# Kernel optimization log

Measured on AMD Instinct MI355X. Metric: run time of the kernel, lower is better.

## Reference

```python
import jax, jax.numpy as jnp
import numpy as np
import math

D = 1024
H = 16
DH = D // H


def sinusoidal_pe(length, d):
    pos = jnp.arange(length, dtype=jnp.float32)[:, None]            # [S,1]
    div = jnp.exp(jnp.arange(0, d, 2, dtype=jnp.float32) * (-math.log(10000.0) / d))  # [d/2]
    ang = pos * div                                                  # [S,d/2]
    # interleave sin (even idx) and cos (odd idx)
    return jnp.stack([jnp.sin(ang), jnp.cos(ang)], axis=-1).reshape(length, d)


def setup_inputs() -> dict:
    key = jax.random.key(0)
    ks = jax.random.split(key, 12)
    s = 0.02
    x = jax.random.normal(ks[0], (2, 2048, D), dtype=jnp.float32)
    return {
        "x": x,
        "ln_g": jnp.ones((D,), jnp.float32),
        "ln_b": jnp.zeros((D,), jnp.float32),
        "Wq": jax.random.normal(ks[1], (D, D), jnp.float32) * s,
        "bq": jnp.zeros((D,), jnp.float32),
        "Wk": jax.random.normal(ks[2], (D, D), jnp.float32) * s,
        "bk": jnp.zeros((D,), jnp.float32),
        "Wv": jax.random.normal(ks[3], (D, D), jnp.float32) * s,
        "bv": jnp.zeros((D,), jnp.float32),
        "Wp": jax.random.normal(ks[4], (D, D), jnp.float32) * s,
        "Wo": jax.random.normal(ks[5], (D, D), jnp.float32) * s,
        "bo": jnp.zeros((D,), jnp.float32),
        "u_bias": jax.random.normal(ks[6], (H, DH), jnp.float32) * 0.05,
        "v_bias": jax.random.normal(ks[7], (H, DH), jnp.float32) * 0.05,
    }


def _relative_shift(pos_score):
    # pos_score: [B,H,S,S]
    B, Hh, S1, S2 = pos_score.shape
    padded = jnp.concatenate([jnp.zeros((B, Hh, S1, 1), pos_score.dtype), pos_score], axis=-1)
    padded = padded.reshape(B, Hh, S2 + 1, S1)
    return padded[:, :, 1:].reshape(B, Hh, S1, S2)


def reference(x, ln_g, ln_b, Wq, bq, Wk, bk, Wv, bv, Wp, Wo, bo, u_bias, v_bias):
    B, S, Dm = x.shape
    dh = Dm // H
    scale = dh ** -0.5

    pe = sinusoidal_pe(S, Dm)                                        # [S,D]

    mu = jnp.mean(x, axis=-1, keepdims=True)
    var = jnp.var(x, axis=-1, keepdims=True)
    xn = (x - mu) / jnp.sqrt(var + 1e-5) * ln_g + ln_b

    q = (xn @ Wq + bq).reshape(B, S, H, dh)                          # [B,S,H,dh]
    k = (xn @ Wk + bk).reshape(B, S, H, dh)
    v = (xn @ Wv + bv).reshape(B, S, H, dh)
    p = (pe @ Wp).reshape(S, H, dh)                                  # [S,H,dh]

    content = jnp.einsum('bihd,bjhd->bhij', q + u_bias, k)
    pos = jnp.einsum('bihd,jhd->bhij', q + v_bias, p)
    pos = _relative_shift(pos)

    attn = jax.nn.softmax((content + pos) * scale, axis=-1)          # [B,H,S,S]
    head = jnp.einsum('bhij,bjhd->bihd', attn, v).reshape(B, S, Dm)
    return head @ Wo + bo
```

## Files before the change

### kernel.cpp

```cpp
#include <hip/hip_runtime.h>
#include <hip/hip_bf16.h>
#include <math.h>

#define Dm   1024
#define Hh   16
#define Sx   2048

typedef short s16x8 __attribute__((ext_vector_type(8)));
typedef float f32x4 __attribute__((ext_vector_type(4)));
typedef unsigned short u16;
typedef u16 u16x4 __attribute__((ext_vector_type(4)));

#if defined(__has_builtin)
#  if __has_builtin(__builtin_amdgcn_cvt_pk_bf16_f32)
#    define HAVE_PKBF16 1
typedef __bf16 bfv2 __attribute__((ext_vector_type(2)));
#  endif
#  if __has_builtin(__builtin_amdgcn_exp2f)
#    define EXP2(x) __builtin_amdgcn_exp2f(x)
#  endif
#endif
#ifndef EXP2
#  define EXP2(x) exp2f(x)
#endif

#define ATT_SCALE 0.1803368801111204f

__device__ __forceinline__ float wave_sum64(float v) {
#pragma unroll
    for (int o = 32; o > 0; o >>= 1) v += __shfl_xor(v, o, 64);
    return v;
}
__device__ __forceinline__ u16 f2bf(float x) {
    unsigned int u = __float_as_uint(x);
    unsigned int r = u + 0x7FFFu + ((u >> 16) & 1u);
    return (u16)(r >> 16);
}
__device__ __forceinline__ float bf2f(u16 h) {
    return __uint_as_float(((unsigned int)h) << 16);
}

__global__ __launch_bounds__(256) void ln_kernel(const float* __restrict__ x,
                                                 const float* __restrict__ g,
                                                 const float* __restrict__ b,
                                                 u16* __restrict__ out16) {
    int row = blockIdx.x;
    int tid = threadIdx.x;
    const float4* xr = (const float4*)(x + (size_t)row * Dm);
    float4 v = xr[tid];
    float s  = v.x + v.y + v.z + v.w;
    float ss = v.x * v.x + v.y * v.y + v.z * v.z + v.w * v.w;
    __shared__ float rbuf[8];
    s  = wave_sum64(s);
    ss = wave_sum64(ss);
    if ((tid & 63) == 0) { rbuf[tid >> 6] = s; rbuf[4 + (tid >> 6)] = ss; }
    __syncthreads();
    float mean = (rbuf[0] + rbuf[1] + rbuf[2] + rbuf[3]) * (1.0f / Dm);
    float msq  = (rbuf[4] + rbuf[5] + rbuf[6] + rbuf[7]) * (1.0f / Dm);
    float var  = msq - mean * mean;
    float rstd = 1.0f / sqrtf(var + 1e-5f);
    float4 gg = ((const float4*)g)[tid];
    float4 bb = ((const float4*)b)[tid];
    float o[4];
    o[0] = (v.x - mean) * rstd * gg.x + bb.x;
    o[1] = (v.y - mean) * rstd * gg.y + bb.y;
    o[2] = (v.z - mean) * rstd * gg.z + bb.z;
    o[3] = (v.w - mean) * rstd * gg.w + bb.w;
    u16x4 hi, lo;
#pragma unroll
    for (int i = 0; i < 4; i++) {
        u16 h = f2bf(o[i]);
        hi[i] = h;
        lo[i] = f2bf(o[i] - bf2f(h));
    }
    *(u16x4*)&out16[(size_t)row * 2048 + tid * 4]        = hi;
    *(u16x4*)&out16[(size_t)row * 2048 + 1024 + tid * 4] = lo;
}

__global__ __launch_bounds__(256) void pe_kernel(u16* __restrict__ pe16) {
    int idx = blockIdx.x * 256 + threadIdx.x;
    int r = idx >> 9;
    int t = idx & 511;
    double div = exp((double)(2 * t) * (-9.210340371976184 / 1024.0));
    double ang = (double)r * div;
    float sv = (float)sin(ang), cv = (float)cos(ang);
    u16 sh = f2bf(sv), chh = f2bf(cv);
    u16* row = pe16 + (size_t)r * 2048;
    row[2 * t]            = sh;
    row[2 * t + 1]        = chh;
    row[1024 + 2 * t]     = f2bf(sv - bf2f(sh));
    row[1024 + 2 * t + 1] = f2bf(cv - bf2f(chh));
}

__global__ __launch_bounds__(256) void wconv_kernel(const float* __restrict__ W0,
                                                    const float* __restrict__ W1,
                                                    const float* __restrict__ W2,
                                                    const float* __restrict__ W3,
                                                    const float* __restrict__ W4,
                                                    u16* __restrict__ WT) {
    int wz = blockIdx.z;
    const float* W = (wz == 0) ? W0 : (wz == 1) ? W1 : (wz == 2) ? W2 : (wz == 3) ? W3 : W4;
    u16* T = WT + (size_t)wz * 1024 * 2048;
    __shared__ float tile[32][33];
    int n0 = blockIdx.x * 32, k0 = blockIdx.y * 32;
    int tx = threadIdx.x & 31, ty = threadIdx.x >> 5;
#pragma unroll
    for (int r = 0; r < 32; r += 8)
        tile[ty + r][tx] = W[(size_t)(k0 + ty + r) * 1024 + n0 + tx];
    __syncthreads();
#pragma unroll
    for (int r = 0; r < 32; r += 8) {
        int n = ty + r;
        float x = tile[tx][n];
        u16 h = f2bf(x);
        float rem = x - bf2f(h);
        T[(size_t)(n0 + n) * 2048 + k0 + tx]        = h;
        T[(size_t)(n0 + n) * 2048 + 1024 + k0 + tx] = f2bf(rem);
    }
}

__global__ __launch_bounds__(256, 4) void gemm_bf16x3(const u16* __restrict__ A16,
                                                      const u16* __restrict__ WT,
                                                      const float* __restrict__ bias,
                                                      float cscale,
                                                      float* __restrict__ C,
                                                      u16* __restrict__ Cb, int M) {
    const int K = 1024, N = 1024;
    __shared__ __align__(16) u16 Ah[64 * 72];
    __shared__ __align__(16) u16 Bh[128 * 72];
    int tid = threadIdx.x;
    int bn = blockIdx.x * 128, bm = blockIdx.y * 64;
    int ar = tid >> 2, ac = (tid & 3) * 8;
    int br = tid >> 1, bs = (tid & 1);
    int w = tid >> 6, ln = tid & 63, g = ln >> 4, l15 = ln & 15;
    int wm = (w & 1) * 32, wn = (w >> 1) * 64;

    const u16* Ap = A16 + (size_t)(bm + ar) * 2048 + ac;
    const u16* Bp = WT + (size_t)(bn + br) * 2048 + bs * 1024;
    u16* Aw = &Ah[ar * 72 + ac];
    u16* Bw = &Bh[br * 72 + bs * 32];

    f32x4 acc[2][4] = {};
    s16x8 pah = *(const s16x8*)Ap;
    s16x8 pal = *(const s16x8*)(Ap + 1024);
    s16x8 pb0 = *(const s16x8*)Bp;
    s16x8 pb1 = *(const s16x8*)(Bp + 8);
    s16x8 pb2 = *(const s16x8*)(Bp + 16);
    s16x8 pb3 = *(const s16x8*)(Bp + 24);

    for (int k0 = 0; k0 < K; k0 += 32) {
        __syncthreads();
        *(s16x8*)Aw        = pah;
        *(s16x8*)(Aw + 32) = pal;
        *(s16x8*)Bw        = pb0;
        *(s16x8*)(Bw + 8)  = pb1;
        *(s16x8*)(Bw + 16) = pb2;
        *(s16x8*)(Bw + 24) = pb3;
        int kn = k0 + 32;
        if (kn < K) {
            pah = *(const s16x8*)(Ap + kn);
            pal = *(const s16x8*)(Ap + 1024 + kn);
            pb0 = *(const s16x8*)(Bp + kn);
            pb1 = *(const s16x8*)(Bp + kn + 8);
            pb2 = *(const s16x8*)(Bp + kn + 16);
            pb3 = *(const s16x8*)(Bp + kn + 24);
        }
        __syncthreads();
        s16x8 ah0 = *(const s16x8*)&Ah[(wm + l15) * 72 + g * 8];
        s16x8 al0 = *(const s16x8*)&Ah[(wm + l15) * 72 + 32 + g * 8];
        s16x8 ah1 = *(const s16x8*)&Ah[(wm + 16 + l15) * 72 + g * 8];
        s16x8 al1 = *(const s16x8*)&Ah[(wm + 16 + l15) * 72 + 32 + g * 8];
#pragma unroll
        for (int nt = 0; nt < 4; nt++) {
            int n = (wn + 16 * nt + l15) * 72;
            s16x8 bh = *(const s16x8*)&Bh[n + g * 8];
            s16x8 bl = *(const s16x8*)&Bh[n + 32 + g * 8];
            acc[0][nt] = __builtin_amdgcn_mfma_f32_16x16x32_bf16(ah0, bh, acc[0][nt], 0, 0, 0);
            acc[0][nt] = __builtin_amdgcn_mfma_f32_16x16x32_bf16(al0, bh, acc[0][nt], 0, 0, 0);
            acc[0][nt] = __builtin_amdgcn_mfma_f32_16x16x32_bf16(ah0, bl, acc[0][nt], 0, 0, 0);
            acc[1][nt] = __builtin_amdgcn_mfma_f32_16x16x32_bf16(ah1, bh, acc[1][nt], 0, 0, 0);
            acc[1][nt] = __builtin_amdgcn_mfma_f32_16x16x32_bf16(al1, bh, acc[1][nt], 0, 0, 0);
            acc[1][nt] = __builtin_amdgcn_mfma_f32_16x16x32_bf16(ah1, bl, acc[1][nt], 0, 0, 0);
        }
    }

    float bv[4];
#pragma unroll
    for (int nt = 0; nt < 4; nt++)
        bv[nt] = bias ? bias[bn + wn + 16 * nt + l15] : 0.0f;
#pragma unroll
    for (int mt = 0; mt < 2; mt++)
#pragma unroll
        for (int r = 0; r < 4; r++) {
            int row = bm + wm + 16 * mt + g * 4 + r;
            if (Cb) {
                u16* cp = Cb + (size_t)row * N + bn + wn + l15;
#pragma unroll
                for (int nt = 0; nt < 4; nt++)
                    cp[16 * nt] = f2bf((acc[mt][nt][r] + bv[nt]) * cscale);
            } else {
                float* cp = C + (size_t)row * N + bn + wn + l15;
#pragma unroll
                for (int nt = 0; nt < 4; nt++)
                    cp[16 * nt] = (acc[mt][nt][r] + bv[nt]) * cscale;
            }
        }
}

__global__ __launch_bounds__(256) void vtrans_kernel(const u16* __restrict__ v,
                                                     u16* __restrict__ vT) {
    __shared__ u16 L[32 * 72];
    int jt = blockIdx.x, h = blockIdx.y, b = blockIdx.z;
    int tid = threadIdx.x;
    int row = tid >> 3, cc = tid & 7;
    const u16* src = v + ((size_t)(b * Sx + jt * 32 + row)) * Dm + h * 64 + cc * 8;
    *(s16x8*)&L[row * 72 + cc * 8] = *(const s16x8*)src;
    __syncthreads();
    int d = tid >> 2, jq = tid & 3;
    s16x8 o;
#pragma unroll
    for (int jj = 0; jj < 8; jj++) o[jj] = (short)L[(jq * 8 + jj) * 72 + d];
    u16* dst = vT + (((size_t)(b * 16 + h) * 64 + jt)) * 2048 + d * 32 + jq * 8;
    *(s16x8*)dst = o;
}

__global__ __launch_bounds__(256) void ukvb_kernel(const u16* __restrict__ k,
                                                   const u16* __restrict__ pp,
                                                   const float* __restrict__ u,
                                                   const float* __restrict__ vb,
                                                   float* __restrict__ ukg,
                                                   float* __restrict__ vbg) {
    int jid = blockIdx.x * 256 + threadIdx.x;
    const u16* src; const float* vec; float* dst; int idx;
    if (jid < 2 * Hh * Sx) {
        int j = jid & 2047, h = (jid >> 11) & 15, b = jid >> 15;
        src = k + ((size_t)(b * Sx + j)) * Dm + h * 64;
        vec = u + h * 64; dst = ukg; idx = jid;
    } else {
        int j2 = jid - 2 * Hh * Sx;
        int r = j2 & 2047, h = j2 >> 11;
        src = pp + (size_t)r * Dm + h * 64;
        vec = vb + h * 64; dst = vbg; idx = j2;
    }
    float s = 0.0f;
#pragma unroll
    for (int c = 0; c < 8; c++) {
        s16x8 kk = *(const s16x8*)(src + c * 8);
#pragma unroll
        for (int i = 0; i < 8; i++) s += bf2f((u16)kk[i]) * vec[c * 8 + i];
    }
    dst[idx] = s;
}

__device__ __forceinline__ void wfill2(s16x8 a0, s16x8 a1, const u16* PW,
                                       int g, int l15, f32x4& d0, f32x4& d1) {
    f32x4 z = {0.f, 0.f, 0.f, 0.f};
    s16x8 b00 = *(const s16x8*)&PW[l15 * 72 + g * 8];
    s16x8 b01 = *(const s16x8*)&PW[l15 * 72 + 32 + g * 8];
    s16x8 b10 = *(const s16x8*)&PW[(16 + l15) * 72 + g * 8];
    s16x8 b11 = *(const s16x8*)&PW[(16 + l15) * 72 + 32 + g * 8];
    d0 = __builtin_amdgcn_mfma_f32_16x16x32_bf16(a0, b00, z, 0, 0, 0);
    d0 = __builtin_amdgcn_mfma_f32_16x16x32_bf16(a1, b01, d0, 0, 0, 0);
    d1 = __builtin_amdgcn_mfma_f32_16x16x32_bf16(a0, b10, z, 0, 0, 0);
    d1 = __builtin_amdgcn_mfma_f32_16x16x32_bf16(a1, b11, d1, 0, 0, 0);
}

__device__ __forceinline__ void window_fill(s16x8 aq0, s16x8 aq1, s16x8 ab0, s16x8 ab1,
                                            const u16* PW, float* Ws,
                                            const float* __restrict__ vbb,
                                            int vstart, int sb, int rbase, int g, int l15) {
    f32x4 e0, e1;
    if (vstart + 31 <= Sx) {
        wfill2(aq0, aq1, PW, g, l15, e0, e1);
    } else if (vstart > Sx) {
        wfill2(ab0, ab1, PW, g, l15, e0, e1);
    } else {
        f32x4 d0, d1, f0, f1;
        wfill2(aq0, aq1, PW, g, l15, d0, d1);
        wfill2(ab0, ab1, PW, g, l15, f0, f1);
        int v0 = vstart + l15, v1 = vstart + 16 + l15;
#pragma unroll
        for (int r = 0; r < 4; r++) {
            e0[r] = (v0 > Sx) ? f0[r] : d0[r];
            e1[r] = (v1 > Sx) ? f1[r] : d1[r];
        }
    }
    int v0 = vstart + l15, v1 = vstart + 16 + l15;
    int pc0 = v0 < Sx ? v0 : v0 - Sx - 1;
    int pc1 = v1 < Sx ? v1 : v1 - Sx - 1;
    float vb0 = (v0 == Sx) ? 0.0f : vbb[pc0];
    float vb1 = (v1 == Sx) ? 0.0f : vbb[pc1];
    int bs = sb + rbase;
#pragma unroll
    for (int r = 0; r < 4; r++) {
        int b2 = bs + r; if (b2 >= 96) b2 -= 96;
        int sl0 = b2 + l15; if (sl0 >= 96) sl0 -= 96;
        int sl1 = sl0 + 16; if (sl1 >= 96) sl1 -= 96;
        Ws[(rbase + r) * 98 + sl0] = (v0 == Sx) ? 0.0f : e0[r] + vb0;
        Ws[(rbase + r) * 98 + sl1] = (v1 == Sx) ? 0.0f : e1[r] + vb1;
    }
}

__global__ __launch_bounds__(256, 4) void flash_kernel(const u16* __restrict__ q,
                                                       const u16* __restrict__ k,
                                                       const u16* __restrict__ vt,
                                                       const u16* __restrict__ pp,
                                                       const float* __restrict__ ukg,
                                                       const float* __restrict__ vbg,
                                                       u16* __restrict__ head16) {
    __shared__ __align__(16) unsigned char smem[39424];
    float* Ws = (float*)smem;
    u16*   Qs = (u16*)smem;
    u16*   Kt = (u16*)(smem + 25088);
    u16*   PW = (u16*)(smem + 29696);
    u16*   PA = (u16*)(smem + 34304);

    int tid = threadIdx.x, blk = blockIdx.x;
    int grp = (blk & 7) + 8 * (blk >> 8);
    int it  = (blk >> 3) & 31;
    int h = grp & 15, b = grp >> 4;
    int i0 = it * 64;
    int a0 = 1984 - i0;

    const u16* qb  = q  + ((size_t)b * Sx) * Dm + h * 64;
    const u16* kb  = k  + ((size_t)b * Sx) * Dm + h * 64;
    const u16* vtb = vt + ((size_t)(b * 16 + h) * 64) * 2048;
    const u16* ppb = pp + h * 64;
    const float* ukb = ukg + (size_t)(b * Hh + h) * Sx;
    const float* vbb = vbg + (size_t)h * Sx;

    int w = tid >> 6, ln = tid & 63, g = ln >> 4, l15 = ln & 15;
    int rv = tid >> 3, ch = tid & 7;
    int rbase = 16 * w + 4 * g;

    for (int c = tid; c < 65 * 8; c += 256) {
        int row = c >> 3, cc = c & 7;
        int i = i0 + row;
        s16x8 tv = {0, 0, 0, 0, 0, 0, 0, 0};
        if (i < Sx) tv = *(const s16x8*)(qb + (size_t)i * Dm + cc * 8);
        *(s16x8*)&Qs[row * 72 + cc * 8] = tv;
    }
    __syncthreads();

    s16x8 aq0 = *(const s16x8*)&Qs[(16 * w + l15) * 72 + g * 8];
    s16x8 aq1 = *(const s16x8*)&Qs[(16 * w + l15) * 72 + 32 + g * 8];
    s16x8 ab0 = *(const s16x8*)&Qs[(16 * w + 1 + l15) * 72 + g * 8];
    s16x8 ab1 = *(const s16x8*)&Qs[(16 * w + 1 + l15) * 72 + 32 + g * 8];
    __syncthreads();

    for (int f = 0; f < 3; f++) {
        int vrb = f * 32;
        if (f) __syncthreads();
        {
            int vv = a0 + vrb + rv;
            s16x8 tv = {0, 0, 0, 0, 0, 0, 0, 0};
            if (vv != Sx) {
                int pc = vv < Sx ? vv : vv - Sx - 1;
                tv = *(const s16x8*)(ppb + (size_t)pc * Dm + ch * 8);
            }
            *(s16x8*)&PW[rv * 72 + ch * 8] = tv;
        }
        __syncthreads();
        window_fill(aq0, aq1, ab0, ab1, PW, Ws, vbb, a0 + vrb, vrb, rbase, g, l15);
    }

    f32x4 O[4] = {{0.f,0.f,0.f,0.f},{0.f,0.f,0.f,0.f},{0.f,0.f,0.f,0.f},{0.f,0.f,0.f,0.f}};
    float m_w = -1e30f;
    float l_i[4] = {0.f, 0.f, 0.f, 0.f};
    int wro[4];
#pragma unroll
    for (int r = 0; r < 4; r++) wro[r] = (rbase + r) * 98;
    int sb = 0;
    int jm = 63;
    int cw = (g >= 2) ? 16 : 0;
    int crd = (l15 >> 3) << 4;
    int pard = (16 * w + l15) * 40 + ((g * 8 + crd) & 31);

    const u16* pK = kb + (size_t)rv * Dm + ch * 8;
    const u16* pV = vtb + l15 * 32 + g * 8;
    s16x8 rK = *(const s16x8*)pK;
    s16x8 rPW = {0, 0, 0, 0, 0, 0, 0, 0};

    for (int t = 0; t < 64; t++) {
        int j0 = t * 32;
        __syncthreads();
        *(s16x8*)&Kt[rv * 72 + ch * 8] = rK;
        if (t >= 1) *(s16x8*)&PW[rv * 72 + ch * 8] = rPW;

        s16x8 bv0 = *(const s16x8*)(pV);
        s16x8 bv1 = *(const s16x8*)(pV + 512);
        s16x8 bv2 = *(const s16x8*)(pV + 1024);
        s16x8 bv3 = *(const s16x8*)(pV + 1536);
        pV += 2048;

        pK += 32 * Dm;
        rK = *(const s16x8*)pK;
        {
            int vv = a0 + (t + 3) * 32 + rv;
            s16x8 z8 = {0, 0, 0, 0, 0, 0, 0, 0};
            if (vv != Sx) {
                int pc = vv < Sx ? vv : vv - Sx - 1;
                if (pc > Sx - 1) pc = Sx - 1;
                z8 = *(const s16x8*)(ppb + (size_t)pc * Dm + ch * 8);
            }
            rPW = z8;
        }
        float uk0 = ukb[j0 + l15];
        float uk1 = ukb[j0 + 16 + l15];
        __syncthreads();

        f32x4 s0, s1;
        {
            f32x4 z = {0.f, 0.f, 0.f, 0.f};
            s16x8 bk00 = *(const s16x8*)&Kt[l15 * 72 + g * 8];
            s16x8 bk01 = *(const s16x8*)&Kt[l15 * 72 + 32 + g * 8];
            s16x8 bk10 = *(const s16x8*)&Kt[(16 + l15) * 72 + g * 8];
            s16x8 bk11 = *(const s16x8*)&Kt[(16 + l15) * 72 + 32 + g * 8];
            s0 = __builtin_amdgcn_mfma_f32_16x16x32_bf16(aq0, bk00, z, 0, 0, 0);
            s0 = __builtin_amdgcn_mfma_f32_16x16x32_bf16(aq1, bk01, s0, 0, 0, 0);
            s1 = __builtin_amdgcn_mfma_f32_16x16x32_bf16(aq0, bk10, z, 0, 0, 0);
            s1 = __builtin_amdgcn_mfma_f32_16x16x32_bf16(aq1, bk11, s1, 0, 0, 0);
        }

        if (t >= 1) {
            window_fill(aq0, aq1, ab0, ab1, PW, Ws, vbb, a0 + j0 + 64, sb, rbase, g, l15);
            sb += 32; if (sb >= 96) sb -= 96;
        }

        int si0 = jm + l15; if (si0 >= 96) si0 -= 96;
        int si1 = si0 + 16; if (si1 >= 96) si1 -= 96;
        jm += 32; if (jm >= 96) jm -= 96;
        float lg0[4], lg1[4];
#pragma unroll
        for (int r = 0; r < 4; r++) {
            lg0[r] = s0[r] + uk0 + Ws[wro[r] + si0];
            lg1[r] = s1[r] + uk1 + Ws[wro[r] + si1];
        }
        float pmax = fmaxf(fmaxf(fmaxf(lg0[0], lg1[0]), fmaxf(lg0[1], lg1[1])),
                           fmaxf(fmaxf(lg0[2], lg1[2]), fmaxf(lg0[3], lg1[3])));
        if (__any(pmax > m_w + 8.0f)) {
            float mx = pmax;
#pragma unroll
            for (int o = 1; o < 64; o <<= 1) mx = fmaxf(mx, __shfl_xor(mx, o, 64));
            float alpha = EXP2(m_w - mx);
            m_w = mx;
            l_i[0] *= alpha; l_i[1] *= alpha; l_i[2] *= alpha; l_i[3] *= alpha;
#pragma unroll
            for (int nt = 0; nt < 4; nt++)
#pragma unroll
                for (int r = 0; r < 4; r++) O[nt][r] *= alpha;
        }
        int c0 = l15 + cw;
        int c1 = l15 + 16 - cw;
#pragma unroll
        for (int r = 0; r < 4; r++) {
            float e0v = EXP2(lg0[r] - m_w);
            float e1v = EXP2(lg1[r] - m_w);
            l_i[r] += e0v + e1v;
#ifdef HAVE_PKBF16
            bfv2 pk2 = __builtin_amdgcn_cvt_pk_bf16_f32(e0v, e1v);
            PA[(rbase + r) * 40 + c0] = __builtin_bit_cast(u16, pk2[0]);
            PA[(rbase + r) * 40 + c1] = __builtin_bit_cast(u16, pk2[1]);
#else
            PA[(rbase + r) * 40 + c0] = f2bf(e0v);
            PA[(rbase + r) * 40 + c1] = f2bf(e1v);
#endif
        }

        {
            s16x8 ap = *(const s16x8*)&PA[pard];
            O[0] = __builtin_amdgcn_mfma_f32_16x16x32_bf16(ap, bv0, O[0], 0, 0, 0);
            O[1] = __builtin_amdgcn_mfma_f32_16x16x32_bf16(ap, bv1, O[1], 0, 0, 0);
            O[2] = __builtin_amdgcn_mfma_f32_16x16x32_bf16(ap, bv2, O[2], 0, 0, 0);
            O[3] = __builtin_amdgcn_mfma_f32_16x16x32_bf16(ap, bv3, O[3], 0, 0, 0);
        }
    }

#pragma unroll
    for (int r = 0; r < 4; r++) {
        float l = l_i[r];
#pragma unroll
        for (int o = 1; o < 16; o <<= 1) l += __shfl_xor(l, o, 64);
        float inv = 1.0f / l;
        int grow = i0 + rbase + r;
        u16* dst = head16 + (size_t)(b * Sx + grow) * 2048 + h * 64 + l15;
#pragma unroll
        for (int nt = 0; nt < 4; nt++) {
            float f = O[nt][r] * inv;
            u16 hh = f2bf(f);
            dst[16 * nt]        = hh;
            dst[1024 + 16 * nt] = f2bf(f - bf2f(hh));
        }
    }
}

extern "C" void kernel_launch(void* const* d_in, const int* in_sizes, int n_in,
                              void* d_out, int out_size, void* d_ws, size_t ws_size,
                              hipStream_t stream) {
    const float* x    = (const float*)d_in[0];
    const float* ln_g = (const float*)d_in[1];
    const float* ln_b = (const float*)d_in[2];
    const float* Wq   = (const float*)d_in[3];
    const float* bq   = (const float*)d_in[4];
    const float* Wk   = (const float*)d_in[5];
    const float* bk   = (const float*)d_in[6];
    const float* Wv   = (const float*)d_in[7];
    const float* bv   = (const float*)d_in[8];
    const float* Wp   = (const float*)d_in[9];
    const float* Wo   = (const float*)d_in[10];
    const float* bo   = (const float*)d_in[11];
    const float* ub   = (const float*)d_in[12];
    const float* vbias= (const float*)d_in[13];

    float* out = (float*)d_out;
    u16* base  = (u16*)d_ws;

    const int MROWS = 2 * Sx;
    u16* xn16   = base;
    u16* head16 = base + 8u  * 1024 * 1024;
    u16* pe16   = base + 16u * 1024 * 1024;
    u16* qb16   = base + 20u * 1024 * 1024;
    u16* kb16   = base + 24u * 1024 * 1024;
    u16* vb16   = base + 28u * 1024 * 1024;
    u16* pp16   = base + 32u * 1024 * 1024;
    u16* vT16   = base + 34u * 1024 * 1024;
    u16* WT     = base + 38u * 1024 * 1024;
    float* ukg  = (float*)(base + 48u * 1024 * 1024);
    float* vbg  = ukg + 2 * Hh * Sx;

    ln_kernel<<<MROWS, 256, 0, stream>>>(x, ln_g, ln_b, xn16);
    pe_kernel<<<Sx * 512 / 256, 256, 0, stream>>>(pe16);

    dim3 gw(32, 32, 5);
    wconv_kernel<<<gw, 256, 0, stream>>>(Wq, Wk, Wv, Wp, Wo, WT);

    dim3 g1(8, MROWS / 64);
    dim3 g2(8, Sx / 64);
    gemm_bf16x3<<<g1, 256, 0, stream>>>(xn16, WT + 0u * 1024 * 2048, bq, 1.0f,      nullptr, qb16, MROWS);
    gemm_bf16x3<<<g1, 256, 0, stream>>>(xn16, WT + 1u * 1024 * 2048, bk, ATT_SCALE, nullptr, kb16, MROWS);
    gemm_bf16x3<<<g1, 256, 0, stream>>>(xn16, WT + 2u * 1024 * 2048, bv, 1.0f,      nullptr, vb16, MROWS);
    gemm_bf16x3<<<g2, 256, 0, stream>>>(pe16, WT + 3u * 1024 * 2048, nullptr, ATT_SCALE, nullptr, pp16, Sx);

    dim3 gv(Sx / 32, Hh, 2);
    vtrans_kernel<<<gv, 256, 0, stream>>>(vb16, vT16);

    ukvb_kernel<<<(2 * Hh * Sx + Hh * Sx) / 256, 256, 0, stream>>>(kb16, pp16, ub, vbias, ukg, vbg);

    flash_kernel<<<2 * Hh * 32, 256, 0, stream>>>(qb16, kb16, vT16, pp16, ukg, vbg, head16);

    gemm_bf16x3<<<g1, 256, 0, stream>>>(head16, WT + 4u * 1024 * 2048, bo, 1.0f, out, nullptr, MROWS);
}
```

Before: 454.2 us.

## Use 128x128 GEMM tiles and merge Q/K/V/P projections into one launch

Replaces the 64x128-tile split-bf16 GEMM with a 128x128-tile version in which each wave computes a 64x64 sub-tile. This doubles operand reuse per LDS load. The four projection GEMMs (Q, K, V from the normed input and P from the positional encoding) now run as one 896-block launch that decodes its block index into the weight, bias, scale and output slab. This removes three launches and fills the GPU better. The larger tile raises register use and lowers occupancy (launch bounds now allow 3 blocks per SM), and the output projection gets only 256 blocks.

```diff
diff --git a/kernel.cpp b/kernel.cpp
--- a/kernel.cpp
+++ b/kernel.cpp
@@ -38,6 +38,9 @@
 }
 __device__ __forceinline__ float bf2f(u16 h) {
     return __uint_as_float(((unsigned int)h) << 16);
+}
+__device__ __forceinline__ f32x4 mfma16(s16x8 a, s16x8 b, f32x4 c) {
+    return __builtin_amdgcn_mfma_f32_16x16x32_bf16(a, b, c, 0, 0, 0);
 }
 
 __global__ __launch_bounds__(256) void ln_kernel(const float* __restrict__ x,
@@ -119,92 +122,124 @@
     }
 }
 
-__global__ __launch_bounds__(256, 4) void gemm_bf16x3(const u16* __restrict__ A16,
-                                                      const u16* __restrict__ WT,
-                                                      const float* __restrict__ bias,
-                                                      float cscale,
-                                                      float* __restrict__ C,
-                                                      u16* __restrict__ Cb, int M) {
-    const int K = 1024, N = 1024;
-    __shared__ __align__(16) u16 Ah[64 * 72];
+__global__ __launch_bounds__(256, 3) void gemm128(const u16* __restrict__ A,
+                                                  const u16* __restrict__ A2,
+                                                  const u16* __restrict__ WT,
+                                                  const float* __restrict__ b0,
+                                                  const float* __restrict__ b1,
+                                                  const float* __restrict__ b2,
+                                                  u16* __restrict__ Cb,
+                                                  float* __restrict__ C,
+                                                  int mode) {
+    __shared__ __align__(16) u16 Ah[128 * 72];
     __shared__ __align__(16) u16 Bh[128 * 72];
     int tid = threadIdx.x;
-    int bn = blockIdx.x * 128, bm = blockIdx.y * 64;
-    int ar = tid >> 2, ac = (tid & 3) * 8;
-    int br = tid >> 1, bs = (tid & 1);
+    int gx, gy, widx;
+    const u16* Asrc = A;
+    if (mode == 0) {
+        int bid = blockIdx.x;
+        if (bid < 768) { gx = bid % 24; gy = bid / 24; widx = gx >> 3; gx &= 7; }
+        else           { int r2 = bid - 768; gx = r2 & 7; gy = r2 >> 3; widx = 3; Asrc = A2; }
+    } else {
+        gx = blockIdx.x; gy = blockIdx.y; widx = 4;
+    }
+    int bn = gx * 128, bm = gy * 128;
+    const u16* Wb = WT + (size_t)widx * (1024 * 2048);
+    const float* bias = (widx == 0) ? b0 : (widx == 1) ? b1 : (widx == 2) ? b2
+                      : (widx == 4) ? b0 : nullptr;
+    float csc = (widx == 1 || widx == 3) ? ATT_SCALE : 1.0f;
+
     int w = tid >> 6, ln = tid & 63, g = ln >> 4, l15 = ln & 15;
-    int wm = (w & 1) * 32, wn = (w >> 1) * 64;
-
-    const u16* Ap = A16 + (size_t)(bm + ar) * 2048 + ac;
-    const u16* Bp = WT + (size_t)(bn + br) * 2048 + bs * 1024;
-    u16* Aw = &Ah[ar * 72 + ac];
-    u16* Bw = &Bh[br * 72 + bs * 32];
-
-    f32x4 acc[2][4] = {};
-    s16x8 pah = *(const s16x8*)Ap;
-    s16x8 pal = *(const s16x8*)(Ap + 1024);
-    s16x8 pb0 = *(const s16x8*)Bp;
-    s16x8 pb1 = *(const s16x8*)(Bp + 8);
-    s16x8 pb2 = *(const s16x8*)(Bp + 16);
-    s16x8 pb3 = *(const s16x8*)(Bp + 24);
-
-    for (int k0 = 0; k0 < K; k0 += 32) {
+    int wm = (w & 1) * 64, wn = (w >> 1) * 64;
+
+    int srow = tid >> 3, c8 = tid & 7;
+    int half = c8 >> 2, cIn = c8 & 3;
+    const u16* Agp = Asrc + (size_t)(bm + srow) * 2048 + half * 1024 + cIn * 8;
+    const u16* Bgp = Wb   + (size_t)(bn + srow) * 2048 + half * 1024 + cIn * 8;
+    u16* Aw = &Ah[srow * 72 + half * 32 + cIn * 8];
+    u16* Bw = &Bh[srow * 72 + half * 32 + cIn * 8];
+
+    f32x4 acc[4][4] = {};
+
+    s16x8 pa0 = *(const s16x8*)(Agp);
+    s16x8 pa1 = *(const s16x8*)(Agp + 65536);
+    s16x8 pa2 = *(const s16x8*)(Agp + 131072);
+    s16x8 pa3 = *(const s16x8*)(Agp + 196608);
+    s16x8 pb0 = *(const s16x8*)(Bgp);
+    s16x8 pb1 = *(const s16x8*)(Bgp + 65536);
+    s16x8 pb2 = *(const s16x8*)(Bgp + 131072);
+    s16x8 pb3 = *(const s16x8*)(Bgp + 196608);
+
+    for (int k0 = 0; k0 < 1024; k0 += 32) {
         __syncthreads();
-        *(s16x8*)Aw        = pah;
-        *(s16x8*)(Aw + 32) = pal;
-        *(s16x8*)Bw        = pb0;
-        *(s16x8*)(Bw + 8)  = pb1;
-        *(s16x8*)(Bw + 16) = pb2;
-        *(s16x8*)(Bw + 24) = pb3;
+        *(s16x8*)(Aw)           = pa0;
+        *(s16x8*)(Aw + 32 * 72) = pa1;
+        *(s16x8*)(Aw + 64 * 72) = pa2;
+        *(s16x8*)(Aw + 96 * 72) = pa3;
+        *(s16x8*)(Bw)           = pb0;
+        *(s16x8*)(Bw + 32 * 72) = pb1;
+        *(s16x8*)(Bw + 64 * 72) = pb2;
+        *(s16x8*)(Bw + 96 * 72) = pb3;
         int kn = k0 + 32;
-        if (kn < K) {
-            pah = *(const s16x8*)(Ap + kn);
-            pal = *(const s16x8*)(Ap + 1024 + kn);
-            pb0 = *(const s16x8*)(Bp + kn);
-            pb1 = *(const s16x8*)(Bp + kn + 8);
-            pb2 = *(const s16x8*)(Bp + kn + 16);
-            pb3 = *(const s16x8*)(Bp + kn + 24);
-        }
+        pa0 = *(const s16x8*)(Agp + kn);
+        pa1 = *(const s16x8*)(Agp + 65536 + kn);
+        pa2 = *(const s16x8*)(Agp + 131072 + kn);
+        pa3 = *(const s16x8*)(Agp + 196608 + kn);
+        pb0 = *(const s16x8*)(Bgp + kn);
+        pb1 = *(const s16x8*)(Bgp + 65536 + kn);
+        pb2 = *(const s16x8*)(Bgp + 131072 + kn);
+        pb3 = *(const s16x8*)(Bgp + 196608 + kn);
         __syncthreads();
-        s16x8 ah0 = *(const s16x8*)&Ah[(wm + l15) * 72 + g * 8];
-        s16x8 al0 = *(const s16x8*)&Ah[(wm + l15) * 72 + 32 + g * 8];
-        s16x8 ah1 = *(const s16x8*)&Ah[(wm + 16 + l15) * 72 + g * 8];
-        s16x8 al1 = *(const s16x8*)&Ah[(wm + 16 + l15) * 72 + 32 + g * 8];
+
+        s16x8 bhf[4], blf[4];
 #pragma unroll
         for (int nt = 0; nt < 4; nt++) {
-            int n = (wn + 16 * nt + l15) * 72;
-            s16x8 bh = *(const s16x8*)&Bh[n + g * 8];
-            s16x8 bl = *(const s16x8*)&Bh[n + 32 + g * 8];
-            acc[0][nt] = __builtin_amdgcn_mfma_f32_16x16x32_bf16(ah0, bh, acc[0][nt], 0, 0, 0);
-            acc[0][nt] = __builtin_amdgcn_mfma_f32_16x16x32_bf16(al0, bh, acc[0][nt], 0, 0, 0);
-            acc[0][nt] = __builtin_amdgcn_mfma_f32_16x16x32_bf16(ah0, bl, acc[0][nt], 0, 0, 0);
-            acc[1][nt] = __builtin_amdgcn_mfma_f32_16x16x32_bf16(ah1, bh, acc[1][nt], 0, 0, 0);
-            acc[1][nt] = __builtin_amdgcn_mfma_f32_16x16x32_bf16(al1, bh, acc[1][nt], 0, 0, 0);
-            acc[1][nt] = __builtin_amdgcn_mfma_f32_16x16x32_bf16(ah1, bl, acc[1][nt], 0, 0, 0);
-        }
-    }
-
-    float bv[4];
+            int br = (wn + nt * 16 + l15) * 72;
+            bhf[nt] = *(const s16x8*)&Bh[br + g * 8];
+            blf[nt] = *(const s16x8*)&Bh[br + 32 + g * 8];
+        }
+#pragma unroll
+        for (int mt = 0; mt < 4; mt++) {
+            int ar = (wm + mt * 16 + l15) * 72;
+            s16x8 ah = *(const s16x8*)&Ah[ar + g * 8];
+            s16x8 al = *(const s16x8*)&Ah[ar + 32 + g * 8];
+#pragma unroll
+            for (int nt = 0; nt < 4; nt++) {
+                acc[mt][nt] = mfma16(ah, bhf[nt], acc[mt][nt]);
+                acc[mt][nt] = mfma16(al, bhf[nt], acc[mt][nt]);
+                acc[mt][nt] = mfma16(ah, blf[nt], acc[mt][nt]);
+            }
+        }
+    }
+
+    float bv4[4];
 #pragma unroll
     for (int nt = 0; nt < 4; nt++)
-        bv[nt] = bias ? bias[bn + wn + 16 * nt + l15] : 0.0f;
-#pragma unroll
-    for (int mt = 0; mt < 2; mt++)
-#pragma unroll
-        for (int r = 0; r < 4; r++) {
-            int row = bm + wm + 16 * mt + g * 4 + r;
-            if (Cb) {
-                u16* cp = Cb + (size_t)row * N + bn + wn + l15;
+        bv4[nt] = bias ? bias[bn + wn + nt * 16 + l15] : 0.0f;
+    if (mode == 0) {
+        u16* Co = Cb + (size_t)widx * (4096 * 1024);
+#pragma unroll
+        for (int mt = 0; mt < 4; mt++)
+#pragma unroll
+            for (int r = 0; r < 4; r++) {
+                int row = bm + wm + mt * 16 + g * 4 + r;
+                u16* cp = Co + (size_t)row * 1024 + bn + wn + l15;
 #pragma unroll
                 for (int nt = 0; nt < 4; nt++)
-                    cp[16 * nt] = f2bf((acc[mt][nt][r] + bv[nt]) * cscale);
-            } else {
-                float* cp = C + (size_t)row * N + bn + wn + l15;
+                    cp[16 * nt] = f2bf((acc[mt][nt][r] + bv4[nt]) * csc);
+            }
+    } else {
+#pragma unroll
+        for (int mt = 0; mt < 4; mt++)
+#pragma unroll
+            for (int r = 0; r < 4; r++) {
+                int row = bm + wm + mt * 16 + g * 4 + r;
+                float* cp = C + (size_t)row * 1024 + bn + wn + l15;
 #pragma unroll
                 for (int nt = 0; nt < 4; nt++)
-                    cp[16 * nt] = (acc[mt][nt][r] + bv[nt]) * cscale;
+                    cp[16 * nt] = acc[mt][nt][r] + bv4[nt];
             }
-        }
+    }
 }
 
 __global__ __launch_bounds__(256) void vtrans_kernel(const u16* __restrict__ v,
@@ -534,12 +569,7 @@
     dim3 gw(32, 32, 5);
     wconv_kernel<<<gw, 256, 0, stream>>>(Wq, Wk, Wv, Wp, Wo, WT);
 
-    dim3 g1(8, MROWS / 64);
-    dim3 g2(8, Sx / 64);
-    gemm_bf16x3<<<g1, 256, 0, stream>>>(xn16, WT + 0u * 1024 * 2048, bq, 1.0f,      nullptr, qb16, MROWS);
-    gemm_bf16x3<<<g1, 256, 0, stream>>>(xn16, WT + 1u * 1024 * 2048, bk, ATT_SCALE, nullptr, kb16, MROWS);
-    gemm_bf16x3<<<g1, 256, 0, stream>>>(xn16, WT + 2u * 1024 * 2048, bv, 1.0f,      nullptr, vb16, MROWS);
-    gemm_bf16x3<<<g2, 256, 0, stream>>>(pe16, WT + 3u * 1024 * 2048, nullptr, ATT_SCALE, nullptr, pp16, Sx);
+    gemm128<<<896, 256, 0, stream>>>(xn16, pe16, WT, bq, bk, bv, qb16, nullptr, 0);
 
     dim3 gv(Sx / 32, Hh, 2);
     vtrans_kernel<<<gv, 256, 0, stream>>>(vb16, vT16);
@@ -548,5 +578,5 @@
 
     flash_kernel<<<2 * Hh * 32, 256, 0, stream>>>(qb16, kb16, vT16, pp16, ukg, vbg, head16);
 
-    gemm_bf16x3<<<g1, 256, 0, stream>>>(head16, WT + 4u * 1024 * 2048, bo, 1.0f, out, nullptr, MROWS);
-}
+    gemm128<<<dim3(8, 32), 256, 0, stream>>>(head16, nullptr, WT, bo, nullptr, nullptr, nullptr, out, 1);
+}
```

Result: faster. 405.3 us (-10.8%).
